# Performance work log

Measured on AMD Instinct MI355X. Metric: run time of the kernel, lower is better.

The kernel has to match this reference:

```python
import jax, jax.numpy as jnp
import numpy as np

N = 65536    # nodes per node type
E = 1048576  # edges per edge type
D = 512      # feature dim
B = 64       # graphs in batch


def _ln(x, g, b):
    m = x.mean(-1, keepdims=True)
    v = ((x - m) ** 2).mean(-1, keepdims=True)
    return (x - m) / jnp.sqrt(v + 1e-5) * g + b


def _seg_softmax(logits, seg, n):
    m = jax.ops.segment_max(logits, seg, num_segments=n)
    e = jnp.exp(logits - m[seg])
    s = jax.ops.segment_sum(e, seg, num_segments=n)
    return e / s[seg]


def setup_inputs():
    key = jax.random.key(0)
    k = jax.random.split(key, 16)
    sc = 1.0 / np.sqrt(D)
    d = {}
    d["x_inst"] = jax.random.normal(k[0], (N, D), jnp.float32)
    d["x_net"] = jax.random.normal(k[1], (N, D), jnp.float32)
    d["ln_g_inst"] = jnp.ones((D,), jnp.float32)
    d["ln_b_inst"] = jnp.zeros((D,), jnp.float32)
    d["ln_g_net"] = jnp.ones((D,), jnp.float32)
    d["ln_b_net"] = jnp.zeros((D,), jnp.float32)
    d["Wkqv_inst"] = jax.random.normal(k[2], (D, 3), jnp.float32) * sc
    d["bkqv_inst"] = jnp.zeros((3,), jnp.float32)
    d["Wkqv_net"] = jax.random.normal(k[3], (D, 3), jnp.float32) * sc
    d["bkqv_net"] = jnp.zeros((3,), jnp.float32)
    d["k_rel_w"] = jax.random.normal(k[4], (2,), jnp.float32)
    d["k_rel_b"] = jnp.zeros((2,), jnp.float32)
    d["v_rel_w"] = jax.random.normal(k[5], (2,), jnp.float32)
    d["v_rel_b"] = jnp.zeros((2,), jnp.float32)
    d["p_rel"] = jnp.ones((2,), jnp.float32)  # per-edge-type attention prior (heads=1)
    d["w_out_inst"] = jax.random.normal(k[6], (), jnp.float32)
    d["b_out_inst"] = jnp.zeros((), jnp.float32)
    d["w_out_net"] = jax.random.normal(k[7], (), jnp.float32)
    d["b_out_net"] = jnp.zeros((), jnp.float32)
    d["W_mlp_inst"] = jax.random.normal(k[8], (2 * D, D), jnp.float32) / np.sqrt(2 * D)
    d["b_mlp_inst"] = jnp.zeros((D,), jnp.float32)
    d["W_mlp_net"] = jax.random.normal(k[9], (2 * D, D), jnp.float32) / np.sqrt(2 * D)
    d["b_mlp_net"] = jnp.zeros((D,), jnp.float32)
    d["ei_i2n"] = jax.random.randint(k[10], (2, E), 0, N)
    d["ei_n2i"] = jax.random.randint(k[11], (2, E), 0, N)
    d["batch_inst"] = jnp.sort(jax.random.randint(k[12], (N,), 0, B))
    d["batch_net"] = jnp.sort(jax.random.randint(k[13], (N,), 0, B))
    return d


def _forward(x_inst, x_net, ln_g_inst, ln_b_inst, ln_g_net, ln_b_net,
             Wkqv_inst, bkqv_inst, Wkqv_net, bkqv_net,
             k_rel_w, k_rel_b, v_rel_w, v_rel_b, p_rel,
             w_out_inst, b_out_inst, w_out_net, b_out_net,
             W_mlp_inst, b_mlp_inst, W_mlp_net, b_mlp_net,
             ei_i2n, ei_n2i, batch_inst, batch_net):
    # LayerNorm per node over features
    xn_i = _ln(x_inst, ln_g_inst, ln_b_inst)
    xn_n = _ln(x_net, ln_g_net, ln_b_net)

    # HGTConv with out_channels=1, heads=1, head_dim=1: kqv are scalar per node
    kqv_i = xn_i @ Wkqv_inst + bkqv_inst  # [N, 3]
    kqv_n = xn_n @ Wkqv_net + bkqv_net
    k_i, q_i, v_i = kqv_i[:, 0], kqv_i[:, 1], kqv_i[:, 2]
    k_n, q_n, v_n = kqv_n[:, 0], kqv_n[:, 1], kqv_n[:, 2]

    def het_attn(k_src, v_src, q_dst, ei, rel):
        src, dst = ei[0], ei[1]
        kt = k_src * k_rel_w[rel] + k_rel_b[rel]  # per-relation K transform
        vt = v_src * v_rel_w[rel] + v_rel_b[rel]  # per-relation V transform
        # head_dim = 1 -> sqrt(D_head) = 1
        logits = q_dst[dst] * kt[src] * p_rel[rel]
        a = _seg_softmax(logits, dst, N)  # segment softmax over incoming edges
        return jax.ops.segment_sum(a * vt[src], dst, num_segments=N)  # [N]

    aggr_net = het_attn(k_i, v_i, q_n, ei_i2n, 0)   # edge type 0: inst -> net
    aggr_inst = het_attn(k_n, v_n, q_i, ei_n2i, 1)  # edge type 1: net -> inst

    # out_lin (1->1) + GELU; skip connection is skipped since 1 != D
    score_inst = jax.nn.gelu(aggr_inst * w_out_inst + b_out_inst, approximate=False)
    score_net = jax.nn.gelu(aggr_net * w_out_net + b_out_net, approximate=False)

    def pool(xn, score, batch, W, b):
        s = _seg_softmax(score, batch, B)              # softmax of scores per graph
        xw = xn * s[:, None]                           # [N, D]
        x_add = jax.ops.segment_sum(xw, batch, num_segments=B)
        x_max = jax.ops.segment_max(xw, batch, num_segments=B)
        return jnp.concatenate([x_add, x_max], axis=-1) @ W + b  # [B, D]

    out_inst = pool(xn_i, score_inst, batch_inst, W_mlp_inst, b_mlp_inst)
    out_net = pool(xn_n, score_net, batch_net, W_mlp_net, b_mlp_net)
    return jnp.concatenate([out_inst, out_net], axis=-1)  # [B, 2*D]


def reference(x_inst, x_net, ln_g_inst, ln_b_inst, ln_g_net, ln_b_net,
              Wkqv_inst, bkqv_inst, Wkqv_net, bkqv_net,
              k_rel_w, k_rel_b, v_rel_w, v_rel_b, p_rel,
              w_out_inst, b_out_inst, w_out_net, b_out_net,
              W_mlp_inst, b_mlp_inst, W_mlp_net, b_mlp_net,
              ei_i2n, ei_n2i, batch_inst, batch_net):
    return _forward(x_inst, x_net, ln_g_inst, ln_b_inst, ln_g_net, ln_b_net,
                    Wkqv_inst, bkqv_inst, Wkqv_net, bkqv_net,
                    k_rel_w, k_rel_b, v_rel_w, v_rel_b, p_rel,
                    w_out_inst, b_out_inst, w_out_net, b_out_net,
                    W_mlp_inst, b_mlp_inst, W_mlp_net, b_mlp_net,
                    ei_i2n, ei_n2i, batch_inst, batch_net)
```

## Files before the change

kernel.cpp:

```cpp
#include <hip/hip_runtime.h>
#include <math.h>
#include <float.h>

#define NN 65536
#define EE 1048576
#define DD 512
#define BB 64
#define SPLIT 8
#define CAP 4608

__device__ __forceinline__ void fadd(float* p, float v) {
    unsafeAtomicAdd(p, v);
}

__device__ __forceinline__ int lowerb(const int* __restrict__ a, int n, int v) {
    int lo = 0, hi = n;
    while (lo < hi) { int mid = (lo + hi) >> 1; if (a[mid] < v) lo = mid + 1; else hi = mid; }
    return lo;
}

__device__ __forceinline__ float dot4(float4 a, float4 b) {
    return fmaf(a.x, b.x, fmaf(a.y, b.y, fmaf(a.z, b.z, a.w * b.w)));
}

template<int CTRL>
__device__ __forceinline__ float dppadd(float v) {
    union { float f; int i; } u, r;
    u.f = v;
    r.i = __builtin_amdgcn_update_dpp(0, u.i, CTRL, 0xF, 0xF, true);
    return v + r.f;
}
__device__ __forceinline__ float wave_sum63(float v) {
    v = dppadd<0x111>(v);
    v = dppadd<0x112>(v);
    v = dppadd<0x114>(v);
    v = dppadd<0x118>(v);
    v = dppadd<0x142>(v);
    v = dppadd<0x143>(v);
    return v;
}

__global__ __launch_bounds__(512) void prep_kernel(
    const float* __restrict__ g_i, const float* __restrict__ b_i,
    const float* __restrict__ g_n, const float* __restrict__ b_n,
    const float* __restrict__ W_i, const float* __restrict__ bk_i,
    const float* __restrict__ W_n, const float* __restrict__ bk_n,
    float* __restrict__ gw, float* __restrict__ cAB)
{
    int t = blockIdx.x;
    const float* g  = t ? g_n : g_i;
    const float* b  = t ? b_n : b_i;
    const float* W  = t ? W_n : W_i;
    const float* bk = t ? bk_n : bk_i;
    int d = threadIdx.x;
    float gv = g[d], bv = b[d];
    float w0 = W[d * 3 + 0], w1 = W[d * 3 + 1], w2 = W[d * 3 + 2];
    float v0 = gv * w0, v1 = gv * w1, v2 = gv * w2;
    gw[((size_t)t * 3 + 0) * DD + d] = v0;
    gw[((size_t)t * 3 + 1) * DD + d] = v1;
    gw[((size_t)t * 3 + 2) * DD + d] = v2;
    __shared__ float red[8];
    float vals[6] = { v0, v1, v2, bv * w0, bv * w1, bv * w2 };
    #pragma unroll
    for (int c = 0; c < 6; ++c) {
        float v = vals[c];
        #pragma unroll
        for (int o = 32; o; o >>= 1) v += __shfl_xor(v, o);
        if ((d & 63) == 0) red[d >> 6] = v;
        __syncthreads();
        if (d == 0) {
            float sum = 0.0f;
            #pragma unroll
            for (int w = 0; w < 8; ++w) sum += red[w];
            cAB[t * 8 + c] = sum + (c >= 3 ? bk[c - 3] : 0.0f);
        }
        __syncthreads();
    }
}

__global__ __launch_bounds__(256) void ln_kqv_kernel(
    const float* __restrict__ x_i, const float* __restrict__ x_n,
    const float* __restrict__ gw, const float* __restrict__ cAB,
    const float* __restrict__ krw, const float* __restrict__ krb,
    const float* __restrict__ vrw, const float* __restrict__ vrb,
    const float* __restrict__ prel,
    float2* __restrict__ mr_o, float2* __restrict__ ktvt2, float* __restrict__ qp)
{
    const int t  = blockIdx.x >> 13;
    const int nb = blockIdx.x & 8191;
    const float* x = t ? x_n : x_i;
    const int lane = threadIdx.x & 63;
    const int w    = threadIdx.x >> 6;
    const int row0 = nb * 8 + w * 2;

    const float4* xr0 = (const float4*)(x + (size_t)row0 * DD);
    const float4* xr1 = (const float4*)(x + (size_t)(row0 + 1) * DD);
    float4 xa0 = xr0[lane], xb0 = xr0[lane + 64];
    float4 xa1 = xr1[lane], xb1 = xr1[lane + 64];

    const float4* g0 = (const float4*)(gw + ((size_t)t * 3 + 0) * DD);
    const float4* g1 = (const float4*)(gw + ((size_t)t * 3 + 1) * DD);
    const float4* g2 = (const float4*)(gw + ((size_t)t * 3 + 2) * DD);
    float4 w0a = g0[lane], w0b = g0[lane + 64];
    float4 w1a = g1[lane], w1b = g1[lane + 64];
    float4 w2a = g2[lane], w2b = g2[lane + 64];

    const float* c = cAB + t * 8;
    float c0 = c[0], c1 = c[1], c2 = c[2], c3 = c[3], c4 = c[4], c5 = c[5];
    const int relk = t, relq = 1 - t;
    float ksc = krw[relk], kbi = krb[relk];
    float vsc = vrw[relk], vbi = vrb[relk];
    float psc = prel[relq];

    float s0  = xa0.x + xa0.y + xa0.z + xa0.w + xb0.x + xb0.y + xb0.z + xb0.w;
    float ss0 = dot4(xa0, xa0) + dot4(xb0, xb0);
    float p00 = dot4(xa0, w0a) + dot4(xb0, w0b);
    float p01 = dot4(xa0, w1a) + dot4(xb0, w1b);
    float p02 = dot4(xa0, w2a) + dot4(xb0, w2b);
    float s1  = xa1.x + xa1.y + xa1.z + xa1.w + xb1.x + xb1.y + xb1.z + xb1.w;
    float ss1 = dot4(xa1, xa1) + dot4(xb1, xb1);
    float p10 = dot4(xa1, w0a) + dot4(xb1, w0b);
    float p11 = dot4(xa1, w1a) + dot4(xb1, w1b);
    float p12 = dot4(xa1, w2a) + dot4(xb1, w2b);

    s0  = wave_sum63(s0);   s1  = wave_sum63(s1);
    ss0 = wave_sum63(ss0);  ss1 = wave_sum63(ss1);
    p00 = wave_sum63(p00);  p10 = wave_sum63(p10);
    p01 = wave_sum63(p01);  p11 = wave_sum63(p11);
    p02 = wave_sum63(p02);  p12 = wave_sum63(p12);

    if (lane == 63) {
        {
            float mean = s0 * (1.0f / DD);
            float var  = ss0 * (1.0f / DD) - mean * mean;
            float rstd = rsqrtf(var + 1e-5f);
            float kv = rstd * (p00 - mean * c0) + c3;
            float qv = rstd * (p01 - mean * c1) + c4;
            float vv = rstd * (p02 - mean * c2) + c5;
            int gn = t * NN + row0;
            mr_o[gn]  = make_float2(mean, rstd);
            ktvt2[gn] = make_float2(kv * ksc + kbi, vv * vsc + vbi);
            qp[gn]    = qv * psc;
        }
        {
            float mean = s1 * (1.0f / DD);
            float var  = ss1 * (1.0f / DD) - mean * mean;
            float rstd = rsqrtf(var + 1e-5f);
            float kv = rstd * (p10 - mean * c0) + c3;
            float qv = rstd * (p11 - mean * c1) + c4;
            float vv = rstd * (p12 - mean * c2) + c5;
            int gn = t * NN + row0 + 1;
            mr_o[gn]  = make_float2(mean, rstd);
            ktvt2[gn] = make_float2(kv * ksc + kbi, vv * vsc + vbi);
            qp[gn]    = qv * psc;
        }
    }
}

__global__ __launch_bounds__(512) void edge_scatter_kernel(
    const int* __restrict__ ei_i2n, const int* __restrict__ ei_n2i,
    const float* __restrict__ ktvt, const float* __restrict__ qp,
    int* __restrict__ cursor, float2* __restrict__ pay, unsigned char* __restrict__ fb)
{
    __shared__ int hist[256];
    __shared__ int base[256];
    int es = blockIdx.x >> 8;
    int wg = blockIdx.x & 255;
    int tid = threadIdx.x;
    if (tid < 256) hist[tid] = 0;
    __syncthreads();
    const int* ei = es ? ei_n2i : ei_i2n;
    int soff = es ? NN : 0;
    int qoff = es ? 0 : NN;
    int r    = es ? 0 : 1;
    float e_[8], ev_[8]; int br_[8];
    int ebase = wg * 4096;
    #pragma unroll
    for (int j = 0; j < 8; ++j) {
        int idx = ebase + j * 512 + tid;
        int src = ei[idx], dst = ei[EE + idx];
        float2 kv = ((const float2*)ktvt)[soff + src];
        float e = __expf(qp[qoff + dst] * kv.x);
        e_[j] = e; ev_[j] = e * kv.y;
        int bin = dst >> 8;
        int rank = atomicAdd(&hist[bin], 1);
        br_[j] = (bin << 21) | ((dst & 255) << 13) | rank;
    }
    __syncthreads();
    if (tid < 256) {
        int c = hist[tid];
        base[tid] = c ? atomicAdd(&cursor[r * 256 + tid], c) : 0;
    }
    __syncthreads();
    #pragma unroll
    for (int j = 0; j < 8; ++j) {
        int br = br_[j];
        int bin = br >> 21, f = (br >> 13) & 255, rank = br & 8191;
        int slot = base[bin] + rank;
        if (slot < CAP) {
            size_t a = (size_t)(r * 256 + bin) * CAP + slot;
            float2 p; p.x = e_[j]; p.y = ev_[j];
            pay[a] = p;
            fb[a] = (unsigned char)f;
        }
    }
}

__global__ __launch_bounds__(256) void bucket_reduce_kernel(
    const int* __restrict__ cursor, const float2* __restrict__ pay,
    const unsigned char* __restrict__ fb, float2* __restrict__ S)
{
    __shared__ float b0[256], b1[256];
    int r = blockIdx.x >> 8, c = blockIdx.x & 255;
    int tid = threadIdx.x;
    b0[tid] = 0.0f; b1[tid] = 0.0f;
    __syncthreads();
    int cnt = min(cursor[r * 256 + c], CAP);
    size_t bb = (size_t)(r * 256 + c) * CAP;
    for (int i = tid; i < cnt; i += 256) {
        float2 p = pay[bb + i];
        int f = fb[bb + i];
        atomicAdd(&b0[f], p.x);
        atomicAdd(&b1[f], p.y);
    }
    __syncthreads();
    float2 o; o.x = b0[tid]; o.y = b1[tid];
    S[r * NN + c * 256 + tid] = o;
}

__global__ __launch_bounds__(256) void score_bsum_kernel(
    const float2* __restrict__ S,
    const float* __restrict__ wout_i, const float* __restrict__ bout_i,
    const float* __restrict__ wout_n, const float* __restrict__ bout_n,
    const int* __restrict__ batch_i, const int* __restrict__ batch_n,
    float* __restrict__ esc, float* __restrict__ bsum)
{
    __shared__ float lsum[BB];
    int tid = threadIdx.x;
    if (tid < BB) lsum[tid] = 0.0f;
    __syncthreads();
    int idx = blockIdx.x * 256 + tid;
    int t = idx >> 16;
    int n = idx & (NN - 1);
    float2 sv = S[idx];
    float aggr = (sv.x > 0.0f) ? sv.y / sv.x : 0.0f;
    float w  = t ? wout_n[0] : wout_i[0];
    float b0 = t ? bout_n[0] : bout_i[0];
    float z  = fmaf(aggr, w, b0);
    float sc = 0.5f * z * (1.0f + erff(z * 0.70710678118654752440f));
    float e  = __expf(sc);
    esc[idx] = e;
    int bb = t ? batch_n[n] : batch_i[n];
    atomicAdd(&lsum[bb], e);
    __syncthreads();
    if (tid < BB && lsum[tid] != 0.0f) fadd(&bsum[t * BB + tid], lsum[tid]);
}

__global__ __launch_bounds__(512) void pool_kernel(
    const float* __restrict__ x_i, const float* __restrict__ x_n,
    const float* __restrict__ g_i, const float* __restrict__ gbi,
    const float* __restrict__ g_n, const float* __restrict__ gbn,
    const float2* __restrict__ mr_, const float* __restrict__ esc,
    const int* __restrict__ batch_i, const int* __restrict__ batch_n,
    const float* __restrict__ bsum,
    float* __restrict__ addp, float* __restrict__ mxp)
{
    int gi = blockIdx.x;
    int t    = gi >> 9;
    int bi   = gi & 511;
    int b    = bi >> 3;
    int part = bi & (SPLIT - 1);
    const float* x     = t ? x_n : x_i;
    const float* gwp   = t ? g_n : g_i;
    const float* gbp   = t ? gbn : gbi;
    const int*   batch = t ? batch_n : batch_i;
    const float2* mr   = mr_ + (size_t)t * NN;
    const float* es    = esc + (size_t)t * NN;
    int start = lowerb(batch, NN, b);
    int end   = lowerb(batch, NN, b + 1);
    int len   = end - start;
    int chunk = (len + SPLIT - 1) / SPLIT;
    int i0 = start + part * chunk;
    int i1 = min(i0 + chunk, end);
    if (i0 > i1) i1 = i0;
    int tid = threadIdx.x;
    int ro  = tid >> 7;
    int c4  = (tid & 127) << 2;
    float4 gv = *(const float4*)(gwp + c4);
    float4 bv = *(const float4*)(gbp + c4);
    float inv = 1.0f / bsum[t * BB + b];
    float4 acc = make_float4(0.0f, 0.0f, 0.0f, 0.0f);
    float4 amx = make_float4(-FLT_MAX, -FLT_MAX, -FLT_MAX, -FLT_MAX);
    int i = i0;
    for (; i + 8 <= i1; i += 8) {
        int r0 = i + ro, r1 = i + 4 + ro;
        float4 xv0 = *(const float4*)(x + (size_t)r0 * DD + c4);
        float4 xv1 = *(const float4*)(x + (size_t)r1 * DD + c4);
        float w0 = es[r0] * inv; float2 q0 = mr[r0];
        float w1 = es[r1] * inv; float2 q1 = mr[r1];
        float4 v0, v1;
        v0.x = ((xv0.x - q0.x) * q0.y * gv.x + bv.x) * w0;
        v0.y = ((xv0.y - q0.x) * q0.y * gv.y + bv.y) * w0;
        v0.z = ((xv0.z - q0.x) * q0.y * gv.z + bv.z) * w0;
        v0.w = ((xv0.w - q0.x) * q0.y * gv.w + bv.w) * w0;
        v1.x = ((xv1.x - q1.x) * q1.y * gv.x + bv.x) * w1;
        v1.y = ((xv1.y - q1.x) * q1.y * gv.y + bv.y) * w1;
        v1.z = ((xv1.z - q1.x) * q1.y * gv.z + bv.z) * w1;
        v1.w = ((xv1.w - q1.x) * q1.y * gv.w + bv.w) * w1;
        acc.x += v0.x + v1.x; acc.y += v0.y + v1.y;
        acc.z += v0.z + v1.z; acc.w += v0.w + v1.w;
        amx.x = fmaxf(amx.x, fmaxf(v0.x, v1.x));
        amx.y = fmaxf(amx.y, fmaxf(v0.y, v1.y));
        amx.z = fmaxf(amx.z, fmaxf(v0.z, v1.z));
        amx.w = fmaxf(amx.w, fmaxf(v0.w, v1.w));
    }
    for (; i < i1; i += 4) {
        int r = i + ro;
        if (r < i1) {
            float4 xv = *(const float4*)(x + (size_t)r * DD + c4);
            float w = es[r] * inv; float2 q = mr[r];
            float4 v;
            v.x = ((xv.x - q.x) * q.y * gv.x + bv.x) * w;
            v.y = ((xv.y - q.x) * q.y * gv.y + bv.y) * w;
            v.z = ((xv.z - q.x) * q.y * gv.z + bv.z) * w;
            v.w = ((xv.w - q.x) * q.y * gv.w + bv.w) * w;
            acc.x += v.x; acc.y += v.y; acc.z += v.z; acc.w += v.w;
            amx.x = fmaxf(amx.x, v.x); amx.y = fmaxf(amx.y, v.y);
            amx.z = fmaxf(amx.z, v.z); amx.w = fmaxf(amx.w, v.w);
        }
    }
    __shared__ float lad[4][DD];
    __shared__ float lmx[4][DD];
    *(float4*)&lad[ro][c4] = acc;
    *(float4*)&lmx[ro][c4] = amx;
    __syncthreads();
    float a = lad[0][tid] + lad[1][tid] + lad[2][tid] + lad[3][tid];
    float m = fmaxf(fmaxf(lmx[0][tid], lmx[1][tid]), fmaxf(lmx[2][tid], lmx[3][tid]));
    size_t po = ((size_t)(t * BB + b) * SPLIT + part) * DD + tid;
    addp[po] = a;
    mxp[po]  = m;
}

__global__ __launch_bounds__(512) void mlp_kernel(
    const float* __restrict__ addp, const float* __restrict__ mxp,
    const float* __restrict__ Wm_i, const float* __restrict__ bm_i,
    const float* __restrict__ Wm_n, const float* __restrict__ bm_n,
    float* __restrict__ out)
{
    __shared__ float cat[2 * DD];
    __shared__ float psum[8][DD];
    int t = blockIdx.x >> 6;
    int b = blockIdx.x & 63;
    int tid = threadIdx.x;
    size_t pb = (size_t)blockIdx.x * SPLIT * DD + tid;
    float a = 0.0f, m = -FLT_MAX;
    #pragma unroll
    for (int p = 0; p < SPLIT; ++p) {
        a += addp[pb + (size_t)p * DD];
        m = fmaxf(m, mxp[pb + (size_t)p * DD]);
    }
    cat[tid]      = a;
    cat[DD + tid] = m;
    __syncthreads();
    const float* W = t ? Wm_n : Wm_i;
    int w = tid >> 6, lane = tid & 63;
    float acc[8] = {0, 0, 0, 0, 0, 0, 0, 0};
    int k0 = w * 128;
    for (int k = k0; k < k0 + 128; ++k) {
        float c = cat[k];
        #pragma unroll
        for (int j = 0; j < 8; ++j)
            acc[j] = fmaf(c, W[(size_t)k * DD + lane + 64 * j], acc[j]);
    }
    #pragma unroll
    for (int j = 0; j < 8; ++j) psum[w][lane + 64 * j] = acc[j];
    __syncthreads();
    float r = (t ? bm_n : bm_i)[tid];
    #pragma unroll
    for (int wv = 0; wv < 8; ++wv) r += psum[wv][tid];
    out[(size_t)b * (2 * DD) + t * DD + tid] = r;
}

extern "C" void kernel_launch(void* const* d_in, const int* in_sizes, int n_in,
                              void* d_out, int out_size, void* d_ws, size_t ws_size,
                              hipStream_t stream)
{
    const float* x_inst = (const float*)d_in[0];
    const float* x_net  = (const float*)d_in[1];
    const float* lng_i  = (const float*)d_in[2];
    const float* lnb_i  = (const float*)d_in[3];
    const float* lng_n  = (const float*)d_in[4];
    const float* lnb_n  = (const float*)d_in[5];
    const float* Wkqv_i = (const float*)d_in[6];
    const float* bkqv_i = (const float*)d_in[7];
    const float* Wkqv_n = (const float*)d_in[8];
    const float* bkqv_n = (const float*)d_in[9];
    const float* krw    = (const float*)d_in[10];
    const float* krb    = (const float*)d_in[11];
    const float* vrw    = (const float*)d_in[12];
    const float* vrb    = (const float*)d_in[13];
    const float* prel   = (const float*)d_in[14];
    const float* wout_i = (const float*)d_in[15];
    const float* bout_i = (const float*)d_in[16];
    const float* wout_n = (const float*)d_in[17];
    const float* bout_n = (const float*)d_in[18];
    const float* Wm_i   = (const float*)d_in[19];
    const float* bm_i   = (const float*)d_in[20];
    const float* Wm_n   = (const float*)d_in[21];
    const float* bm_n   = (const float*)d_in[22];
    const int* ei_i2n   = (const int*)d_in[23];
    const int* ei_n2i   = (const int*)d_in[24];
    const int* batch_i  = (const int*)d_in[25];
    const int* batch_n  = (const int*)d_in[26];

    float* base   = (float*)d_ws;
    float2* mr    = (float2*)base;
    float* ktvt   = base +  4 * (size_t)NN;
    float* qp     = base +  8 * (size_t)NN;
    float* esc    = base + 10 * (size_t)NN;
    float2* S     = (float2*)(base + 12 * (size_t)NN);
    int*   cursor = (int*)(base + 16 * (size_t)NN);
    float* bsum   = base + 16 * (size_t)NN + 512;
    float* addp   = bsum + 256;
    float* mxp    = addp + 2 * BB * SPLIT * DD;
    float2* pay   = (float2*)(mxp + 2 * BB * SPLIT * DD);
    unsigned char* fbb = (unsigned char*)(pay + 2 * 256 * (size_t)CAP);
    float* gw     = (float*)(fbb + 2 * 256 * (size_t)CAP);
    float* cAB    = gw + 2 * 3 * DD;

    (void)hipMemsetAsync(cursor, 0, (512 + 256) * sizeof(int), stream);

    prep_kernel<<<2, 512, 0, stream>>>(lng_i, lnb_i, lng_n, lnb_n,
        Wkqv_i, bkqv_i, Wkqv_n, bkqv_n, gw, cAB);

    ln_kqv_kernel<<<2 * NN / 8, 256, 0, stream>>>(x_inst, x_net, gw, cAB,
        krw, krb, vrw, vrb, prel, mr, (float2*)ktvt, qp);

    edge_scatter_kernel<<<512, 512, 0, stream>>>(ei_i2n, ei_n2i, ktvt, qp,
        cursor, pay, fbb);

    bucket_reduce_kernel<<<512, 256, 0, stream>>>(cursor, pay, fbb, S);

    score_bsum_kernel<<<2 * NN / 256, 256, 0, stream>>>(S,
        wout_i, bout_i, wout_n, bout_n, batch_i, batch_n, esc, bsum);

    pool_kernel<<<2 * BB * SPLIT, 512, 0, stream>>>(x_inst, x_net,
        lng_i, lnb_i, lng_n, lnb_n, mr, esc, batch_i, batch_n,
        bsum, addp, mxp);

    mlp_kernel<<<2 * BB, 512, 0, stream>>>(addp, mxp, Wm_i, bm_i, Wm_n, bm_n,
        (float*)d_out);
}
```

Baseline: 479.7 us.

## Replace two-pass bucketed edge scatter with direct global atomic accumulation

Drops the histogram-bucket scatter kernel and the bucket-reduce kernel. A single edge kernel now computes the exp-weighted terms and adds them straight into the per-node sum buffer with global float atomics, with S zeroed by a memset. This removes the intermediate payload and byte-index buffers, one launch, and the CAP overflow truncation. In exchange it takes 8M random global atomics, which may contend, and summation order is no longer deterministic.

Result: slower. 624.8 us (+30.2%).

```diff
diff --git a/kernel.cpp b/kernel.cpp
--- a/kernel.cpp
+++ b/kernel.cpp
@@ -7,7 +7,6 @@
 #define DD 512
 #define BB 64
 #define SPLIT 8
-#define CAP 4608
 
 __device__ __forceinline__ void fadd(float* p, float v) {
     unsafeAtomicAdd(p, v);
@@ -157,75 +156,37 @@
     }
 }
 
-__global__ __launch_bounds__(512) void edge_scatter_kernel(
+__global__ __launch_bounds__(256) void edge_attn_kernel(
     const int* __restrict__ ei_i2n, const int* __restrict__ ei_n2i,
     const float* __restrict__ ktvt, const float* __restrict__ qp,
-    int* __restrict__ cursor, float2* __restrict__ pay, unsigned char* __restrict__ fb)
-{
-    __shared__ int hist[256];
-    __shared__ int base[256];
-    int es = blockIdx.x >> 8;
-    int wg = blockIdx.x & 255;
-    int tid = threadIdx.x;
-    if (tid < 256) hist[tid] = 0;
-    __syncthreads();
+    float* __restrict__ S)
+{
+    int es = blockIdx.x >> 10;
+    int wg = blockIdx.x & 1023;
     const int* ei = es ? ei_n2i : ei_i2n;
     int soff = es ? NN : 0;
     int qoff = es ? 0 : NN;
     int r    = es ? 0 : 1;
-    float e_[8], ev_[8]; int br_[8];
-    int ebase = wg * 4096;
-    #pragma unroll
-    for (int j = 0; j < 8; ++j) {
-        int idx = ebase + j * 512 + tid;
-        int src = ei[idx], dst = ei[EE + idx];
-        float2 kv = ((const float2*)ktvt)[soff + src];
-        float e = __expf(qp[qoff + dst] * kv.x);
-        e_[j] = e; ev_[j] = e * kv.y;
-        int bin = dst >> 8;
-        int rank = atomicAdd(&hist[bin], 1);
-        br_[j] = (bin << 21) | ((dst & 255) << 13) | rank;
-    }
-    __syncthreads();
-    if (tid < 256) {
-        int c = hist[tid];
-        base[tid] = c ? atomicAdd(&cursor[r * 256 + tid], c) : 0;
-    }
-    __syncthreads();
-    #pragma unroll
-    for (int j = 0; j < 8; ++j) {
-        int br = br_[j];
-        int bin = br >> 21, f = (br >> 13) & 255, rank = br & 8191;
-        int slot = base[bin] + rank;
-        if (slot < CAP) {
-            size_t a = (size_t)(r * 256 + bin) * CAP + slot;
-            float2 p; p.x = e_[j]; p.y = ev_[j];
-            pay[a] = p;
-            fb[a] = (unsigned char)f;
-        }
-    }
-}
-
-__global__ __launch_bounds__(256) void bucket_reduce_kernel(
-    const int* __restrict__ cursor, const float2* __restrict__ pay,
-    const unsigned char* __restrict__ fb, float2* __restrict__ S)
-{
-    __shared__ float b0[256], b1[256];
-    int r = blockIdx.x >> 8, c = blockIdx.x & 255;
-    int tid = threadIdx.x;
-    b0[tid] = 0.0f; b1[tid] = 0.0f;
-    __syncthreads();
-    int cnt = min(cursor[r * 256 + c], CAP);
-    size_t bb = (size_t)(r * 256 + c) * CAP;
-    for (int i = tid; i < cnt; i += 256) {
-        float2 p = pay[bb + i];
-        int f = fb[bb + i];
-        atomicAdd(&b0[f], p.x);
-        atomicAdd(&b1[f], p.y);
-    }
-    __syncthreads();
-    float2 o; o.x = b0[tid]; o.y = b1[tid];
-    S[r * NN + c * 256 + tid] = o;
+    int e0 = (wg * 256 + threadIdx.x) * 4;
+    int4 s4 = *(const int4*)(ei + e0);
+    int4 d4 = *(const int4*)(ei + EE + e0);
+    const float2* kt = (const float2*)ktvt + soff;
+    const float*  q  = qp + qoff;
+    float* Sb = S + (size_t)r * NN * 2;
+    float2 kv0 = kt[s4.x], kv1 = kt[s4.y], kv2 = kt[s4.z], kv3 = kt[s4.w];
+    float q0 = q[d4.x], q1 = q[d4.y], q2 = q[d4.z], q3 = q[d4.w];
+    float e0_ = __expf(q0 * kv0.x);
+    float e1_ = __expf(q1 * kv1.x);
+    float e2_ = __expf(q2 * kv2.x);
+    float e3_ = __expf(q3 * kv3.x);
+    fadd(&Sb[2 * d4.x],     e0_);
+    fadd(&Sb[2 * d4.x + 1], e0_ * kv0.y);
+    fadd(&Sb[2 * d4.y],     e1_);
+    fadd(&Sb[2 * d4.y + 1], e1_ * kv1.y);
+    fadd(&Sb[2 * d4.z],     e2_);
+    fadd(&Sb[2 * d4.z + 1], e2_ * kv2.y);
+    fadd(&Sb[2 * d4.w],     e3_);
+    fadd(&Sb[2 * d4.w + 1], e3_ * kv3.y);
 }
 
 __global__ __launch_bounds__(256) void score_bsum_kernel(
@@ -418,17 +379,15 @@
     float* ktvt   = base +  4 * (size_t)NN;
     float* qp     = base +  8 * (size_t)NN;
     float* esc    = base + 10 * (size_t)NN;
-    float2* S     = (float2*)(base + 12 * (size_t)NN);
-    int*   cursor = (int*)(base + 16 * (size_t)NN);
-    float* bsum   = base + 16 * (size_t)NN + 512;
+    float* S      = base + 12 * (size_t)NN;
+    float* bsum   = base + 16 * (size_t)NN;
     float* addp   = bsum + 256;
     float* mxp    = addp + 2 * BB * SPLIT * DD;
-    float2* pay   = (float2*)(mxp + 2 * BB * SPLIT * DD);
-    unsigned char* fbb = (unsigned char*)(pay + 2 * 256 * (size_t)CAP);
-    float* gw     = (float*)(fbb + 2 * 256 * (size_t)CAP);
+    float* gw     = mxp  + 2 * BB * SPLIT * DD;
     float* cAB    = gw + 2 * 3 * DD;
 
-    (void)hipMemsetAsync(cursor, 0, (512 + 256) * sizeof(int), stream);
+    (void)hipMemsetAsync(S, 0, 4 * (size_t)NN * sizeof(float), stream);
+    (void)hipMemsetAsync(bsum, 0, 256 * sizeof(float), stream);
 
     prep_kernel<<<2, 512, 0, stream>>>(lng_i, lnb_i, lng_n, lnb_n,
         Wkqv_i, bkqv_i, Wkqv_n, bkqv_n, gw, cAB);
@@ -436,12 +395,9 @@
     ln_kqv_kernel<<<2 * NN / 8, 256, 0, stream>>>(x_inst, x_net, gw, cAB,
         krw, krb, vrw, vrb, prel, mr, (float2*)ktvt, qp);
 
-    edge_scatter_kernel<<<512, 512, 0, stream>>>(ei_i2n, ei_n2i, ktvt, qp,
-        cursor, pay, fbb);
-
-    bucket_reduce_kernel<<<512, 256, 0, stream>>>(cursor, pay, fbb, S);
-
-    score_bsum_kernel<<<2 * NN / 256, 256, 0, stream>>>(S,
+    edge_attn_kernel<<<2048, 256, 0, stream>>>(ei_i2n, ei_n2i, ktvt, qp, S);
+
+    score_bsum_kernel<<<2 * NN / 256, 256, 0, stream>>>((const float2*)S,
         wout_i, bout_i, wout_n, bout_n, batch_i, batch_n, esc, bsum);
 
     pool_kernel<<<2 * BB * SPLIT, 512, 0, stream>>>(x_inst, x_net,
```
